# Kernel optimization log

Hardware: AMD Instinct MI355X
Metric: run time of the kernel (lower is better)

## Reference

```python
import jax, jax.numpy as jnp
import numpy as np

B, S, D = 1, 2048, 2048
NH, NKV, HD = 16, 8, 128
FF = 8192
L = 2
V = 32000
THETA = 10000.0
EPS = 1e-5
SCALE = 0.02


def setup_inputs() -> dict:
    key = jax.random.key(0)
    ks = jax.random.split(key, 16)
    return {
        "input_ids": jax.random.randint(ks[0], (B, S), 0, V, dtype=jnp.int32),
        "embed": jax.random.normal(ks[1], (V, D), jnp.float32) * SCALE,
        "Wq": jax.random.normal(ks[2], (L, D, NH * HD), jnp.float32) * SCALE,
        "Wk": jax.random.normal(ks[3], (L, D, NKV * HD), jnp.float32) * SCALE,
        "Wv": jax.random.normal(ks[4], (L, D, NKV * HD), jnp.float32) * SCALE,
        "Wo": jax.random.normal(ks[5], (L, NH * HD, D), jnp.float32) * SCALE,
        "Wgate": jax.random.normal(ks[6], (L, D, FF), jnp.float32) * SCALE,
        "Wup": jax.random.normal(ks[7], (L, D, FF), jnp.float32) * SCALE,
        "Wdown": jax.random.normal(ks[8], (L, FF, D), jnp.float32) * SCALE,
        "norm_attn": jnp.ones((L, D), jnp.float32),
        "norm_mlp": jnp.ones((L, D), jnp.float32),
        "norm_final": jnp.ones((D,), jnp.float32),
        "lm_head": jax.random.normal(ks[9], (D, V), jnp.float32) * SCALE,
        "D1": jax.random.normal(ks[10], (S,), jnp.float32) + 2.0,
        "D2": jax.random.normal(ks[11], (HD,), jnp.float32) + 2.0,
        "D3": jax.random.normal(ks[12], (S,), jnp.float32) + 2.0,
    }


def _rms_norm(x, w):
    return x * jax.lax.rsqrt(jnp.mean(x * x, axis=-1, keepdims=True) + EPS) * w


def _rotate_half(x):
    x1, x2 = jnp.split(x, 2, axis=-1)
    return jnp.concatenate([-x2, x1], axis=-1)


def _forward(input_ids, embed, Wq, Wk, Wv, Wo, Wgate, Wup, Wdown,
             norm_attn, norm_mlp, norm_final, lm_head, D1, D2, D3):
    # RoPE tables: [1,1,S,HD]
    inv_freq = 1.0 / (THETA ** (jnp.arange(0, HD, 2, dtype=jnp.float32) / HD))
    freqs = jnp.arange(S, dtype=jnp.float32)[:, None] * inv_freq[None, :]
    emb = jnp.concatenate([freqs, freqs], axis=-1)
    cos = jnp.cos(emb)[None, None]
    sin = jnp.sin(emb)[None, None]
    causal = jnp.tril(jnp.ones((S, S), dtype=bool))
    neg = jnp.finfo(jnp.float32).min
    D1i, D2i, D3i = 1.0 / D1, 1.0 / D2, 1.0 / D3
    n_rep = NH // NKV

    h = embed[input_ids]  # [B,S,D]
    for l in range(L):
        # --- attention block ---
        x = _rms_norm(h, norm_attn[l])
        q = (x @ Wq[l]).reshape(B, S, NH, HD).transpose(0, 2, 1, 3)   # [B,NH,S,HD]
        k = (x @ Wk[l]).reshape(B, S, NKV, HD).transpose(0, 2, 1, 3)  # [B,NKV,S,HD]
        v = (x @ Wv[l]).reshape(B, S, NKV, HD).transpose(0, 2, 1, 3)
        q = q * cos + _rotate_half(q) * sin
        k = k * cos + _rotate_half(k) * sin
        # repeat_kv (GQA)
        k = jnp.repeat(k, n_rep, axis=1)
        v = jnp.repeat(v, n_rep, axis=1)
        # TEE diagonal encryption: Q' = D1 Q D2, K'^T = D2^-1 K^T D3
        q_enc = q * D1[None, None, :, None] * D2[None, None, None, :]
        k_enc = k * D3[None, None, :, None] * D2i[None, None, None, :]
        scores = jnp.einsum('bhqd,bhkd->bhqk', q_enc, k_enc)
        # decrypt: D1^-1 (Q'K'^T) D3^-1  (mathematically cancels encryption)
        scores = scores * D1i[None, None, :, None] * D3i[None, None, None, :]
        scores = scores / jnp.sqrt(jnp.float32(HD))
        scores = jnp.where(causal[None, None], scores, neg)
        probs = jax.nn.softmax(scores, axis=-1)
        o = jnp.einsum('bhqk,bhkd->bhqd', probs, v)
        o = o.transpose(0, 2, 1, 3).reshape(B, S, NH * HD)
        h = h + o @ Wo[l]
        # --- SwiGLU MLP block ---
        x = _rms_norm(h, norm_mlp[l])
        h = h + (jax.nn.silu(x @ Wgate[l]) * (x @ Wup[l])) @ Wdown[l]

    h = _rms_norm(h, norm_final)
    return h @ lm_head  # logits [B,S,V]


def reference(input_ids, embed, Wq, Wk, Wv, Wo, Wgate, Wup, Wdown,
              norm_attn, norm_mlp, norm_final, lm_head, D1, D2, D3):
    return _forward(input_ids, embed, Wq, Wk, Wv, Wo, Wgate, Wup, Wdown,
                    norm_attn, norm_mlp, norm_final, lm_head, D1, D2, D3)
```

## Files before the change

kernel.cpp:

```cpp
#include <hip/hip_runtime.h>
#include <cstdint>
#include <cstddef>

typedef __attribute__((ext_vector_type(4))) float f32x4;
typedef __attribute__((ext_vector_type(8))) short short8;
typedef __attribute__((ext_vector_type(4))) unsigned int u32x4;

static const int TS = 2048;
static const int DM = 2048;
static const int NHEAD = 16, NKVH = 8, HDIM = 128;
static const int FFD = 8192;
static const int NVOC = 32000;
static const int QKVN = 4096;

__device__ __forceinline__ unsigned short f2bf(float f){
  unsigned int u = __builtin_bit_cast(unsigned int, f);
  u += 0x7FFFu + ((u >> 16) & 1u);
  return (unsigned short)(u >> 16);
}
__device__ __forceinline__ float bf2f(short h){
  unsigned int u = ((unsigned int)(unsigned short)h) << 16;
  return __builtin_bit_cast(float, u);
}
__device__ __forceinline__ f32x4 mfma16(short8 a, short8 b, f32x4 c){
  return __builtin_amdgcn_mfma_f32_16x16x32_bf16(a, b, c, 0, 0, 0);
}
__device__ __forceinline__ void gload16(const void* g, void* l){
  __builtin_amdgcn_global_load_lds(
      (const __attribute__((address_space(1))) unsigned int*)g,
      (__attribute__((address_space(3))) unsigned int*)l, 16, 0, 0);
}

__global__ void rope_tables_k(float* __restrict__ cosT, float* __restrict__ sinT){
  int idx = blockIdx.x * 256 + threadIdx.x;
  int s = idx >> 6, j = idx & 63;
  float inv = exp2f(-(float)j * (13.287712379549449f / 64.0f));
  float ang = (float)s * inv;
  cosT[idx] = cosf(ang);
  sinT[idx] = sinf(ang);
}

__global__ void embed_k(const int* __restrict__ ids, const float* __restrict__ E,
                        float* __restrict__ h){
  int s = blockIdx.x, tid = threadIdx.x;
  long id = ids[s];
  const f32x4* src = (const f32x4*)(E + id * (long)DM);
  f32x4* dst = (f32x4*)(h + (long)s * DM);
  dst[tid] = src[tid];
  dst[tid + 256] = src[tid + 256];
}

__global__ void rmsnorm_k(const float* __restrict__ x, const float* __restrict__ w,
                          short* __restrict__ out){
  int s = blockIdx.x, tid = threadIdx.x;
  const float* row = x + (long)s * DM;
  f32x4 v0 = *(const f32x4*)&row[tid * 8];
  f32x4 v1 = *(const f32x4*)&row[tid * 8 + 4];
  float ss = v0[0]*v0[0] + v0[1]*v0[1] + v0[2]*v0[2] + v0[3]*v0[3]
           + v1[0]*v1[0] + v1[1]*v1[1] + v1[2]*v1[2] + v1[3]*v1[3];
  #pragma unroll
  for (int off = 32; off; off >>= 1) ss += __shfl_xor(ss, off);
  __shared__ float sred[4];
  int wave = tid >> 6, lane = tid & 63;
  if (lane == 0) sred[wave] = ss;
  __syncthreads();
  float tot = sred[0] + sred[1] + sred[2] + sred[3];
  float r = rsqrtf(tot * (1.0f / (float)DM) + 1e-5f);
  f32x4 w0 = *(const f32x4*)&w[tid * 8];
  f32x4 w1 = *(const f32x4*)&w[tid * 8 + 4];
  short8 o;
  #pragma unroll
  for (int j = 0; j < 4; j++) o[j] = (short)f2bf(v0[j] * r * w0[j]);
  #pragma unroll
  for (int j = 0; j < 4; j++) o[4 + j] = (short)f2bf(v1[j] * r * w1[j]);
  *(short8*)&out[(long)s * DM + tid * 8] = o;
}

__global__ void transpose_k(const float* __restrict__ B, short* __restrict__ Bt,
                            int K, int N){
  __shared__ float t[64][65];
  int tid = threadIdx.x;
  int kb = blockIdx.y * 64, nb = blockIdx.x * 64;
  int r0 = tid >> 4, c4 = tid & 15;
  #pragma unroll
  for (int p = 0; p < 4; p++){
    int r = r0 + p * 16;
    f32x4 v = *(const f32x4*)&B[(long)(kb + r) * N + nb + c4 * 4];
    t[r][c4*4+0] = v[0]; t[r][c4*4+1] = v[1]; t[r][c4*4+2] = v[2]; t[r][c4*4+3] = v[3];
  }
  __syncthreads();
  int n0 = tid >> 3, k0 = (tid & 7) * 8;
  #pragma unroll
  for (int p = 0; p < 2; p++){
    int n = n0 + p * 32;
    short8 o;
    #pragma unroll
    for (int j = 0; j < 8; j++) o[j] = (short)f2bf(t[k0 + j][n]);
    *(short8*)&Bt[(long)(nb + n) * K + kb + k0] = o;
  }
}

__global__ void vtrans_k(const short* __restrict__ vb, short* __restrict__ vtb, int stride){
  int s0 = blockIdx.x * 64, kv = blockIdx.y;
  int tid = threadIdx.x;
  int s = s0 + (tid & 63);
  int d0 = (tid >> 6) * 8;
  #pragma unroll
  for (int p = 0; p < 4; p++){
    int d = d0 + p * 32;
    short8 v = *(const short8*)&vb[(long)s * stride + kv * HDIM + d];
    #pragma unroll
    for (int j = 0; j < 8; j++)
      vtb[(long)(kv * HDIM + d + j) * TS + s] = v[j];
  }
}

__global__ void rope_apply_k(short* __restrict__ buf, const float* __restrict__ cosT,
                             const float* __restrict__ sinT, int nh, int stride, int coloff){
  int idx = blockIdx.x * 256 + threadIdx.x;
  int j = idx & 63;
  int t = idx >> 6;
  int hh = t % nh;
  int s = t / nh;
  long base = (long)s * stride + coloff + hh * HDIM + j;
  float c = cosT[s * 64 + j], sn = sinT[s * 64 + j];
  float x1 = bf2f(buf[base]), x2 = bf2f(buf[base + 64]);
  buf[base]      = (short)f2bf(x1 * c - x2 * sn);
  buf[base + 64] = (short)f2bf(x2 * c + x1 * sn);
}

__global__ void reduce4_k(const float* __restrict__ p, float* __restrict__ h){
  const long stride = (long)TS * DM;
  long i = ((long)blockIdx.x * 256 + threadIdx.x) * 4;
  f32x4 a = *(const f32x4*)&h[i];
  f32x4 v0 = *(const f32x4*)&p[i];
  f32x4 v1 = *(const f32x4*)&p[i + stride];
  f32x4 v2 = *(const f32x4*)&p[i + 2 * stride];
  f32x4 v3 = *(const f32x4*)&p[i + 3 * stride];
  a = a + ((v0 + v1) + (v2 + v3));
  *(f32x4*)&h[i] = a;
}

template<int EPI>
__global__ __launch_bounds__(512, 2)
void gemm256(const short* __restrict__ A, int lda,
             const short* __restrict__ Bt, int ldb,
             float* __restrict__ Cf, short* __restrict__ Cb,
             const short* __restrict__ Xtra, int N, int K){
  __shared__ short lds[4][2][8192];
  const int tid = threadIdx.x;
  const int wid = tid >> 6, lane = tid & 63;
  const int wr = wid >> 2, wc = wid & 3;
  const int fr = lane & 15, fch = lane >> 4;
  const int nt = K >> 5;

  const int z = blockIdx.y;
  A  += (long)z * K;
  Bt += (long)z * K;

  const int nbt = N >> 8;
  const int nwg = nbt << 3;
  const int q = nwg >> 3;
  const int swz = (blockIdx.x & 7) * q + (blockIdx.x >> 3);
  const int mb = swz & 7, nb = swz >> 3;

  const short* Abase = A  + (long)(mb * 256 + fr) * lda + fch * 8;
  const short* Bbase = Bt + (long)(nb * 256 + fr) * ldb + fch * 8;
  const int gA0 = wid * 2, gA1 = wid * 2 + 1;

  short8 aE[4], aO[4], bE[2], bO[2];
  f32x4 acc[8][4] = {};

#define STG_A(bufc, g_, tau_) \
  gload16(Abase + (long)((g_) * 16) * lda + (long)(tau_) * 32, &lds[bufc][0][(g_) * 512])
#define STG_B(bufc, g_, tau_) \
  gload16(Bbase + (long)((g_) * 16) * ldb + (long)(tau_) * 32, &lds[bufc][1][(g_) * 512])
#define RDA(dst, bufc, mh) do{ \
    _Pragma("unroll") \
    for (int j_ = 0; j_ < 4; j_++) \
      dst[j_] = *(const short8*)&lds[bufc][0][(wr * 8 + (mh) * 4 + j_) * 512 + fch * 128 + fr * 8]; \
  }while(0)
#define RDB(dst, bufc, nh) do{ \
    _Pragma("unroll") \
    for (int i_ = 0; i_ < 2; i_++) \
      dst[i_] = *(const short8*)&lds[bufc][1][(wc * 4 + (nh) * 2 + i_) * 512 + fch * 128 + fr * 8]; \
  }while(0)
#define MM8(va, vb, mh, nh) do{ \
    __builtin_amdgcn_s_setprio(1); \
    _Pragma("unroll") \
    for (int j_ = 0; j_ < 4; j_++) \
      _Pragma("unroll") \
      for (int i_ = 0; i_ < 2; i_++) \
        acc[(mh)*4+j_][(nh)*2+i_] = mfma16(va[j_], vb[i_], acc[(mh)*4+j_][(nh)*2+i_]); \
    __builtin_amdgcn_s_setprio(0); \
  }while(0)
#define SB __builtin_amdgcn_sched_barrier(0)

#define TILE(t_, bufR, bufN, bufS, bC, bNx) do{ \
    const int tau_ = ((t_) + 2 < nt) ? (t_) + 2 : nt - 1; \
    RDB(bNx, bufR, 1); STG_A(bufS, gA0, tau_); SB; MM8(aE, bC, 0, 0); \
    RDA(aO,  bufR, 1); STG_A(bufS, gA1, tau_); SB; MM8(aE, bNx, 0, 1); \
    asm volatile("s_waitcnt vmcnt(2)" ::: "memory"); \
    __builtin_amdgcn_s_barrier(); \
    RDA(aE,  bufN, 0); STG_B(bufS, gA0, tau_); SB; MM8(aO, bNx, 1, 1); \
    RDB(bNx, bufN, 0); STG_B(bufS, gA1, tau_); SB; MM8(aO, bC, 1, 0); \
    __builtin_amdgcn_s_barrier(); \
  }while(0)

  STG_A(0, gA0, 0); STG_A(0, gA1, 0); STG_B(0, gA0, 0); STG_B(0, gA1, 0);
  STG_A(1, gA0, 1); STG_A(1, gA1, 1); STG_B(1, gA0, 1); STG_B(1, gA1, 1);
  asm volatile("s_waitcnt vmcnt(4)" ::: "memory");
  __builtin_amdgcn_s_barrier();
  RDA(aE, 0, 0); RDB(bE, 0, 0);

  const int nIter = nt >> 2;
  for (int it = 0; it < nIter; ++it){
    const int t0 = it << 2;
    TILE(t0 + 0, 0, 1, 2, bE, bO);
    TILE(t0 + 1, 1, 2, 3, bO, bE);
    TILE(t0 + 2, 2, 3, 0, bE, bO);
    TILE(t0 + 3, 3, 0, 1, bO, bE);
  }

#undef STG_A
#undef STG_B
#undef RDA
#undef RDB
#undef MM8
#undef SB
#undef TILE

  const int rb0 = mb * 256 + wr * 128 + fch * 4;
  const int cb0 = nb * 256 + wc * 64 + fr;
  const long pbase = (EPI == 5) ? (long)z * ((long)TS * N) : 0;
  #pragma unroll
  for (int m = 0; m < 8; m++)
    #pragma unroll
    for (int n = 0; n < 4; n++)
      #pragma unroll
      for (int i = 0; i < 4; i++){
        long idx = (long)(rb0 + m * 16 + i) * N + (cb0 + n * 16);
        float v = acc[m][n][i];
        if constexpr (EPI == 0) Cf[idx] = v;
        else if constexpr (EPI == 1) Cb[idx] = (short)f2bf(v);
        else if constexpr (EPI == 3){
          float sg = 1.0f / (1.0f + __expf(-v));
          Cb[idx] = (short)f2bf(v * sg);
        } else if constexpr (EPI == 4){
          float g = bf2f(Xtra[idx]);
          Cb[idx] = (short)f2bf(g * v);
        } else {
          Cf[pbase + idx] = v;
        }
      }
}

template<int EPI>
__global__ __launch_bounds__(256)
void gemm_bt(const short* __restrict__ A, const short* __restrict__ Bt,
             float* __restrict__ Cf, short* __restrict__ Cb,
             const short* __restrict__ Xtra, int N, int K){
  __shared__ short As[4096];
  __shared__ short Bs[4096];
  const int tid = threadIdx.x;
  const int wave = tid >> 6, lane = tid & 63;
  const int wr = wave >> 1, wc = wave & 1;
  const int mb = blockIdx.y, nb = blockIdx.x;

  const int srow = lane & 15;
  const int scol = (lane >> 4) * 8;
  const short* ApL0 = A + (long)(mb * 128 + wave * 16 + srow) * K + scol;
  const short* ApL1 = ApL0 + (long)64 * K;
  const short* BpL0 = Bt + (long)(nb * 128 + wave * 16 + srow) * K + scol;
  const short* BpL1 = BpL0 + (long)64 * K;

  f32x4 acc[4][4] = {};
  const int fr = lane & 15, fch = lane >> 4;

  for (int kb = 0; kb < K; kb += 32){
    __syncthreads();
    gload16(ApL0 + kb, &As[wave * 512]);
    gload16(ApL1 + kb, &As[(4 + wave) * 512]);
    gload16(BpL0 + kb, &Bs[wave * 512]);
    gload16(BpL1 + kb, &Bs[(4 + wave) * 512]);
    __syncthreads();
    short8 a[4], b[4];
    #pragma unroll
    for (int m = 0; m < 4; m++)
      a[m] = *(const short8*)&As[(wr * 4 + m) * 512 + fch * 128 + fr * 8];
    #pragma unroll
    for (int n = 0; n < 4; n++)
      b[n] = *(const short8*)&Bs[(wc * 4 + n) * 512 + fch * 128 + fr * 8];
    #pragma unroll
    for (int m = 0; m < 4; m++)
      #pragma unroll
      for (int n = 0; n < 4; n++)
        acc[m][n] = mfma16(a[m], b[n], acc[m][n]);
  }

  const int rb = mb * 128 + wr * 64 + (lane >> 4) * 4;
  const int cb = nb * 128 + wc * 64 + (lane & 15);
  #pragma unroll
  for (int m = 0; m < 4; m++)
    #pragma unroll
    for (int n = 0; n < 4; n++)
      #pragma unroll
      for (int i = 0; i < 4; i++){
        long idx = (long)(rb + m * 16 + i) * N + (cb + n * 16);
        float v = acc[m][n][i];
        if constexpr (EPI == 0) Cf[idx] = v;
        else if constexpr (EPI == 1) Cb[idx] = (short)f2bf(v);
        else if constexpr (EPI == 2) Cf[idx] += v;
        else if constexpr (EPI == 3){
          float sg = 1.0f / (1.0f + __expf(-v));
          Cb[idx] = (short)f2bf(v * sg);
        } else {
          float g = bf2f(Xtra[idx]);
          Cb[idx] = (short)f2bf(g * v);
        }
      }
}

__device__ __forceinline__ int qoff(int r, int cB){ return r * 256 + (cB ^ ((r & 7) << 4)); }
__device__ __forceinline__ int voff(int d, int cB){ return d * 128 + (cB ^ ((d & 7) << 4)); }
__device__ __forceinline__ int poff(int r, int cB){ return r * 128 + (cB ^ ((r & 7) << 4)); }

__global__ __launch_bounds__(256)
void attn_k(const short* __restrict__ qb, const short* __restrict__ kb,
            const short* __restrict__ vtb, short* __restrict__ ob){
  __shared__ short Qs[64 * 128];
  __shared__ short Ks[64 * 128];
  __shared__ short Vt[128 * 64];
  __shared__ short Ps[64 * 64];
  const int tid = threadIdx.x, wave = tid >> 6, lane = tid & 63;
  const int qt = blockIdx.x, head = blockIdx.y, kvh = head >> 1;
  const float scale = 0.08838834764831845f;

  {
    int r0 = tid >> 4, c16 = tid & 15;
    #pragma unroll
    for (int p = 0; p < 4; p++){
      int r = r0 + p * 16;
      u32x4 v = *(const u32x4*)&qb[(long)(qt * 64 + r) * QKVN + head * HDIM + c16 * 8];
      *(u32x4*)((char*)Qs + qoff(r, c16 * 16)) = v;
    }
  }

  float mrun[4] = {-1e30f, -1e30f, -1e30f, -1e30f};
  float lrun[4] = {0.f, 0.f, 0.f, 0.f};
  f32x4 accO[8] = {};

  for (int kt = 0; kt <= qt; kt++){
    __syncthreads();
    {
      int r0 = tid >> 4, c16 = tid & 15;
      #pragma unroll
      for (int p = 0; p < 4; p++){
        int r = r0 + p * 16;
        u32x4 v = *(const u32x4*)&kb[(long)(kt * 64 + r) * QKVN + kvh * HDIM + c16 * 8];
        *(u32x4*)((char*)Ks + qoff(r, c16 * 16)) = v;
      }
      int vr0 = tid >> 3, vc = tid & 7;
      #pragma unroll
      for (int p = 0; p < 4; p++){
        int d = vr0 + p * 32;
        u32x4 v = *(const u32x4*)&vtb[(long)(kvh * HDIM + d) * TS + kt * 64 + vc * 8];
        *(u32x4*)((char*)Vt + voff(d, vc * 16)) = v;
      }
    }
    __syncthreads();

    f32x4 sacc[4] = {};
    #pragma unroll
    for (int k4 = 0; k4 < 4; k4++){
      short8 aq = *(const short8*)((const char*)Qs +
                   qoff(wave * 16 + (lane & 15), k4 * 64 + (lane >> 4) * 16));
      #pragma unroll
      for (int n = 0; n < 4; n++){
        short8 bk = *(const short8*)((const char*)Ks +
                     qoff(n * 16 + (lane & 15), k4 * 64 + (lane >> 4) * 16));
        sacc[n] = mfma16(aq, bk, sacc[n]);
      }
    }

    const bool diag = (kt == qt);
    float mt[4] = {-1e30f, -1e30f, -1e30f, -1e30f};
    #pragma unroll
    for (int n = 0; n < 4; n++)
      #pragma unroll
      for (int i = 0; i < 4; i++){
        float v = sacc[n][i] * scale;
        if (diag){
          int rr = (lane >> 4) * 4 + i + wave * 16;
          int cc = n * 16 + (lane & 15);
          if (cc > rr) v = -1e30f;
        }
        sacc[n][i] = v;
        mt[i] = fmaxf(mt[i], v);
      }
    #pragma unroll
    for (int off = 1; off < 16; off <<= 1)
      #pragma unroll
      for (int i = 0; i < 4; i++) mt[i] = fmaxf(mt[i], __shfl_xor(mt[i], off));
    float alpha[4], rsum[4];
    #pragma unroll
    for (int i = 0; i < 4; i++){
      float mn = fmaxf(mrun[i], mt[i]);
      alpha[i] = __expf(mrun[i] - mn);
      mrun[i] = mn;
      rsum[i] = 0.f;
    }
    #pragma unroll
    for (int n = 0; n < 4; n++)
      #pragma unroll
      for (int i = 0; i < 4; i++){
        float p = __expf(sacc[n][i] - mrun[i]);
        sacc[n][i] = p;
        rsum[i] += p;
      }
    #pragma unroll
    for (int off = 1; off < 16; off <<= 1)
      #pragma unroll
      for (int i = 0; i < 4; i++) rsum[i] += __shfl_xor(rsum[i], off);
    #pragma unroll
    for (int i = 0; i < 4; i++) lrun[i] = lrun[i] * alpha[i] + rsum[i];

    #pragma unroll
    for (int n = 0; n < 4; n++)
      #pragma unroll
      for (int i = 0; i < 4; i++){
        int rr = wave * 16 + (lane >> 4) * 4 + i;
        int cc = n * 16 + (lane & 15);
        *(short*)((char*)Ps + poff(rr, cc * 2)) = (short)f2bf(sacc[n][i]);
      }

    #pragma unroll
    for (int n = 0; n < 8; n++)
      #pragma unroll
      for (int i = 0; i < 4; i++) accO[n][i] *= alpha[i];
    #pragma unroll
    for (int ks = 0; ks < 2; ks++){
      short8 ap = *(const short8*)((const char*)Ps +
                   poff(wave * 16 + (lane & 15), ks * 64 + (lane >> 4) * 16));
      #pragma unroll
      for (int n = 0; n < 8; n++){
        short8 bv = *(const short8*)((const char*)Vt +
                     voff(n * 16 + (lane & 15), ks * 64 + (lane >> 4) * 16));
        accO[n] = mfma16(ap, bv, accO[n]);
      }
    }
  }

  #pragma unroll
  for (int i = 0; i < 4; i++){
    float inv = 1.0f / lrun[i];
    int rr = qt * 64 + wave * 16 + (lane >> 4) * 4 + i;
    #pragma unroll
    for (int n = 0; n < 8; n++){
      int cc = head * HDIM + n * 16 + (lane & 15);
      ob[(long)rr * DM + cc] = (short)f2bf(accO[n][i] * inv);
    }
  }
}

extern "C" void kernel_launch(void* const* d_in, const int* in_sizes, int n_in,
                              void* d_out, int out_size, void* d_ws, size_t ws_size,
                              hipStream_t stream){
  (void)in_sizes; (void)n_in; (void)out_size; (void)ws_size;
  const int*   ids = (const int*)d_in[0];
  const float* E   = (const float*)d_in[1];
  const float* Wq  = (const float*)d_in[2];
  const float* Wk  = (const float*)d_in[3];
  const float* Wv  = (const float*)d_in[4];
  const float* Wo  = (const float*)d_in[5];
  const float* Wg  = (const float*)d_in[6];
  const float* Wu  = (const float*)d_in[7];
  const float* Wd  = (const float*)d_in[8];
  const float* nA  = (const float*)d_in[9];
  const float* nM  = (const float*)d_in[10];
  const float* nF  = (const float*)d_in[11];
  const float* LMH = (const float*)d_in[12];
  float* out = (float*)d_out;

  char* ws = (char*)d_ws;
  size_t off = 0;
  auto alloc = [&](size_t bytes){ void* p = ws + off; off += (bytes + 255) & ~(size_t)255; return p; };
  float* h    = (float*)alloc((size_t)TS * DM * 4);
  short* xb   = (short*)alloc((size_t)TS * DM * 2);
  short* qkvb = (short*)alloc((size_t)TS * QKVN * 2);
  short* vtb  = (short*)alloc((size_t)NKVH * HDIM * TS * 2);
  short* obuf = (short*)alloc((size_t)TS * DM * 2);
  short* sg   = (short*)alloc((size_t)TS * FFD * 2);
  short* actb = (short*)alloc((size_t)TS * FFD * 2);
  float* cosT = (float*)alloc((size_t)TS * 64 * 4);
  float* sinT = (float*)alloc((size_t)TS * 64 * 4);
  short* wT   = (short*)alloc((size_t)NVOC * DM * 2);
  float* pPart = (float*)((char*)wT + (size_t)36 * 1024 * 1024);

  rope_tables_k<<<512, 256, 0, stream>>>(cosT, sinT);
  embed_k<<<TS, 256, 0, stream>>>(ids, E, h);

  for (int l = 0; l < 2; l++){
    rmsnorm_k<<<TS, 256, 0, stream>>>(h, nA + (size_t)l * DM, xb);
    transpose_k<<<dim3(32, 32), 256, 0, stream>>>(Wq + (size_t)l * DM * DM, wT, DM, DM);
    transpose_k<<<dim3(16, 32), 256, 0, stream>>>(Wk + (size_t)l * DM * 1024, wT + (size_t)2048 * DM, DM, 1024);
    transpose_k<<<dim3(16, 32), 256, 0, stream>>>(Wv + (size_t)l * DM * 1024, wT + (size_t)3072 * DM, DM, 1024);
    gemm256<1><<<dim3(128), 512, 0, stream>>>(xb, DM, wT, DM, nullptr, qkvb, nullptr, QKVN, DM);
    rope_apply_k<<<8192, 256, 0, stream>>>(qkvb, cosT, sinT, NHEAD, QKVN, 0);
    rope_apply_k<<<4096, 256, 0, stream>>>(qkvb, cosT, sinT, NKVH, QKVN, 2048);
    vtrans_k<<<dim3(32, 8), 256, 0, stream>>>(qkvb + 3072, vtb, QKVN);
    attn_k<<<dim3(32, 16), 256, 0, stream>>>(qkvb, qkvb + 2048, vtb, obuf);
    transpose_k<<<dim3(32, 32), 256, 0, stream>>>(Wo + (size_t)l * DM * DM, wT, DM, DM);
    gemm_bt<2><<<dim3(16, 16), 256, 0, stream>>>(obuf, wT, h, nullptr, nullptr, DM, DM);
    rmsnorm_k<<<TS, 256, 0, stream>>>(h, nM + (size_t)l * DM, xb);
    transpose_k<<<dim3(128, 32), 256, 0, stream>>>(Wg + (size_t)l * DM * FFD, wT, DM, FFD);
    gemm256<3><<<dim3(256), 512, 0, stream>>>(xb, DM, wT, DM, nullptr, sg, nullptr, FFD, DM);
    transpose_k<<<dim3(128, 32), 256, 0, stream>>>(Wu + (size_t)l * DM * FFD, wT, DM, FFD);
    gemm256<4><<<dim3(256), 512, 0, stream>>>(xb, DM, wT, DM, nullptr, actb, sg, FFD, DM);
    transpose_k<<<dim3(32, 128), 256, 0, stream>>>(Wd + (size_t)l * FFD * DM, wT, FFD, DM);
    gemm256<5><<<dim3(64, 4), 512, 0, stream>>>(actb, FFD, wT, FFD, pPart, nullptr, nullptr, DM, FFD / 4);
    reduce4_k<<<4096, 256, 0, stream>>>(pPart, h);
  }

  rmsnorm_k<<<TS, 256, 0, stream>>>(h, nF, xb);
  transpose_k<<<dim3(500, 32), 256, 0, stream>>>(LMH, wT, DM, NVOC);
  gemm256<0><<<dim3(1000), 512, 0, stream>>>(xb, DM, wT, DM, out, nullptr, nullptr, NVOC, DM);
}
```

Before: 1.546 ms.

## Store GEMM operands in pre-tiled 16x32 bf16 blocks for contiguous loads

Adds a tiled offset function so activations (rmsnorm output, attention output, SwiGLU product) and transposed weights are written as contiguous 16x32 bf16 tiles. The GEMM kernels then load each tile with one fully contiguous 1KB wave-wide global_load_lds instead of 16 strided row segments. This aims to improve global memory coalescing and cut TLB and address-computation cost in the main GEMMs. In exchange, producer stores become scattered in the tiled layout, and every consumer must agree on the layout.

```diff
diff --git a/kernel.cpp b/kernel.cpp
--- a/kernel.cpp
+++ b/kernel.cpp
@@ -29,6 +29,10 @@
   __builtin_amdgcn_global_load_lds(
       (const __attribute__((address_space(1))) unsigned int*)g,
       (__attribute__((address_space(3))) unsigned int*)l, 16, 0, 0);
+}
+__device__ __forceinline__ long toff(int r, int k, int ldk){
+  return ((long)((r >> 4) * ldk + (k >> 5)) << 9)
+       + (((k & 31) >> 3) << 7) + ((r & 15) << 3) + (k & 7);
 }
 
 __global__ void rope_tables_k(float* __restrict__ cosT, float* __restrict__ sinT){
@@ -73,7 +77,7 @@
   for (int j = 0; j < 4; j++) o[j] = (short)f2bf(v0[j] * r * w0[j]);
   #pragma unroll
   for (int j = 0; j < 4; j++) o[4 + j] = (short)f2bf(v1[j] * r * w1[j]);
-  *(short8*)&out[(long)s * DM + tid * 8] = o;
+  *(short8*)&out[toff(s, tid * 8, DM >> 5)] = o;
 }
 
 __global__ void transpose_k(const float* __restrict__ B, short* __restrict__ Bt,
@@ -82,6 +86,7 @@
   int tid = threadIdx.x;
   int kb = blockIdx.y * 64, nb = blockIdx.x * 64;
   int r0 = tid >> 4, c4 = tid & 15;
+  const int ldk = K >> 5;
   #pragma unroll
   for (int p = 0; p < 4; p++){
     int r = r0 + p * 16;
@@ -96,7 +101,7 @@
     short8 o;
     #pragma unroll
     for (int j = 0; j < 8; j++) o[j] = (short)f2bf(t[k0 + j][n]);
-    *(short8*)&Bt[(long)(nb + n) * K + kb + k0] = o;
+    *(short8*)&Bt[toff(nb + n, kb + k0, ldk)] = o;
   }
 }
 
@@ -143,10 +148,10 @@
 
 template<int EPI>
 __global__ __launch_bounds__(512, 2)
-void gemm256(const short* __restrict__ A, int lda,
-             const short* __restrict__ Bt, int ldb,
+void gemm256(const short* __restrict__ A, int ldkA,
+             const short* __restrict__ Bt, int ldkB,
              float* __restrict__ Cf, short* __restrict__ Cb,
-             const short* __restrict__ Xtra, int N, int K){
+             const short* __restrict__ Xtra, int N, int K, int ldkC){
   __shared__ short lds[4][2][8192];
   const int tid = threadIdx.x;
   const int wid = tid >> 6, lane = tid & 63;
@@ -155,8 +160,7 @@
   const int nt = K >> 5;
 
   const int z = blockIdx.y;
-  A  += (long)z * K;
-  Bt += (long)z * K;
+  const int k0 = z * nt;
 
   const int nbt = N >> 8;
   const int nwg = nbt << 3;
@@ -164,17 +168,17 @@
   const int swz = (blockIdx.x & 7) * q + (blockIdx.x >> 3);
   const int mb = swz & 7, nb = swz >> 3;
 
-  const short* Abase = A  + (long)(mb * 256 + fr) * lda + fch * 8;
-  const short* Bbase = Bt + (long)(nb * 256 + fr) * ldb + fch * 8;
+  const short* Abase = A  + ((long)(mb * 16) * ldkA + k0) * 512 + lane * 8;
+  const short* Bbase = Bt + ((long)(nb * 16) * ldkB + k0) * 512 + lane * 8;
   const int gA0 = wid * 2, gA1 = wid * 2 + 1;
 
   short8 aE[4], aO[4], bE[2], bO[2];
   f32x4 acc[8][4] = {};
 
 #define STG_A(bufc, g_, tau_) \
-  gload16(Abase + (long)((g_) * 16) * lda + (long)(tau_) * 32, &lds[bufc][0][(g_) * 512])
+  gload16(Abase + ((long)(g_) * ldkA + (tau_)) * 512, &lds[bufc][0][(g_) * 512])
 #define STG_B(bufc, g_, tau_) \
-  gload16(Bbase + (long)((g_) * 16) * ldb + (long)(tau_) * 32, &lds[bufc][1][(g_) * 512])
+  gload16(Bbase + ((long)(g_) * ldkB + (tau_)) * 512, &lds[bufc][1][(g_) * 512])
 #define RDA(dst, bufc, mh) do{ \
     _Pragma("unroll") \
     for (int j_ = 0; j_ < 4; j_++) \
@@ -239,7 +243,8 @@
     for (int n = 0; n < 4; n++)
       #pragma unroll
       for (int i = 0; i < 4; i++){
-        long idx = (long)(rb0 + m * 16 + i) * N + (cb0 + n * 16);
+        const int rr = rb0 + m * 16 + i, cc = cb0 + n * 16;
+        long idx = (long)rr * N + cc;
         float v = acc[m][n][i];
         if constexpr (EPI == 0) Cf[idx] = v;
         else if constexpr (EPI == 1) Cb[idx] = (short)f2bf(v);
@@ -248,7 +253,7 @@
           Cb[idx] = (short)f2bf(v * sg);
         } else if constexpr (EPI == 4){
           float g = bf2f(Xtra[idx]);
-          Cb[idx] = (short)f2bf(g * v);
+          Cb[toff(rr, cc, ldkC)] = (short)f2bf(g * v);
         } else {
           Cf[pbase + idx] = v;
         }
@@ -257,7 +262,8 @@
 
 template<int EPI>
 __global__ __launch_bounds__(256)
-void gemm_bt(const short* __restrict__ A, const short* __restrict__ Bt,
+void gemm_bt(const short* __restrict__ A, int ldkA,
+             const short* __restrict__ Bt, int ldkB,
              float* __restrict__ Cf, short* __restrict__ Cb,
              const short* __restrict__ Xtra, int N, int K){
   __shared__ short As[4096];
@@ -267,22 +273,19 @@
   const int wr = wave >> 1, wc = wave & 1;
   const int mb = blockIdx.y, nb = blockIdx.x;
 
-  const int srow = lane & 15;
-  const int scol = (lane >> 4) * 8;
-  const short* ApL0 = A + (long)(mb * 128 + wave * 16 + srow) * K + scol;
-  const short* ApL1 = ApL0 + (long)64 * K;
-  const short* BpL0 = Bt + (long)(nb * 128 + wave * 16 + srow) * K + scol;
-  const short* BpL1 = BpL0 + (long)64 * K;
+  const short* Abase = A  + (long)(mb * 8) * ldkA * 512 + lane * 8;
+  const short* Bbase = Bt + (long)(nb * 8) * ldkB * 512 + lane * 8;
 
   f32x4 acc[4][4] = {};
   const int fr = lane & 15, fch = lane >> 4;
-
-  for (int kb = 0; kb < K; kb += 32){
+  const int nt = K >> 5;
+
+  for (int tau = 0; tau < nt; tau++){
     __syncthreads();
-    gload16(ApL0 + kb, &As[wave * 512]);
-    gload16(ApL1 + kb, &As[(4 + wave) * 512]);
-    gload16(BpL0 + kb, &Bs[wave * 512]);
-    gload16(BpL1 + kb, &Bs[(4 + wave) * 512]);
+    gload16(Abase + ((long)wave * ldkA + tau) * 512,       &As[wave * 512]);
+    gload16(Abase + ((long)(wave + 4) * ldkA + tau) * 512, &As[(4 + wave) * 512]);
+    gload16(Bbase + ((long)wave * ldkB + tau) * 512,       &Bs[wave * 512]);
+    gload16(Bbase + ((long)(wave + 4) * ldkB + tau) * 512, &Bs[(4 + wave) * 512]);
     __syncthreads();
     short8 a[4], b[4];
     #pragma unroll
@@ -458,7 +461,7 @@
     #pragma unroll
     for (int n = 0; n < 8; n++){
       int cc = head * HDIM + n * 16 + (lane & 15);
-      ob[(long)rr * DM + cc] = (short)f2bf(accO[n][i] * inv);
+      ob[toff(rr, cc, DM >> 5)] = (short)f2bf(accO[n][i] * inv);
     }
   }
 }
@@ -505,24 +508,24 @@
     transpose_k<<<dim3(32, 32), 256, 0, stream>>>(Wq + (size_t)l * DM * DM, wT, DM, DM);
     transpose_k<<<dim3(16, 32), 256, 0, stream>>>(Wk + (size_t)l * DM * 1024, wT + (size_t)2048 * DM, DM, 1024);
     transpose_k<<<dim3(16, 32), 256, 0, stream>>>(Wv + (size_t)l * DM * 1024, wT + (size_t)3072 * DM, DM, 1024);
-    gemm256<1><<<dim3(128), 512, 0, stream>>>(xb, DM, wT, DM, nullptr, qkvb, nullptr, QKVN, DM);
+    gemm256<1><<<dim3(128), 512, 0, stream>>>(xb, 64, wT, 64, nullptr, qkvb, nullptr, QKVN, DM, 0);
     rope_apply_k<<<8192, 256, 0, stream>>>(qkvb, cosT, sinT, NHEAD, QKVN, 0);
     rope_apply_k<<<4096, 256, 0, stream>>>(qkvb, cosT, sinT, NKVH, QKVN, 2048);
     vtrans_k<<<dim3(32, 8), 256, 0, stream>>>(qkvb + 3072, vtb, QKVN);
     attn_k<<<dim3(32, 16), 256, 0, stream>>>(qkvb, qkvb + 2048, vtb, obuf);
     transpose_k<<<dim3(32, 32), 256, 0, stream>>>(Wo + (size_t)l * DM * DM, wT, DM, DM);
-    gemm_bt<2><<<dim3(16, 16), 256, 0, stream>>>(obuf, wT, h, nullptr, nullptr, DM, DM);
+    gemm_bt<2><<<dim3(16, 16), 256, 0, stream>>>(obuf, 64, wT, 64, h, nullptr, nullptr, DM, DM);
     rmsnorm_k<<<TS, 256, 0, stream>>>(h, nM + (size_t)l * DM, xb);
     transpose_k<<<dim3(128, 32), 256, 0, stream>>>(Wg + (size_t)l * DM * FFD, wT, DM, FFD);
-    gemm256<3><<<dim3(256), 512, 0, stream>>>(xb, DM, wT, DM, nullptr, sg, nullptr, FFD, DM);
+    gemm256<3><<<dim3(256), 512, 0, stream>>>(xb, 64, wT, 64, nullptr, sg, nullptr, FFD, DM, 0);
     transpose_k<<<dim3(128, 32), 256, 0, stream>>>(Wu + (size_t)l * DM * FFD, wT, DM, FFD);
-    gemm256<4><<<dim3(256), 512, 0, stream>>>(xb, DM, wT, DM, nullptr, actb, sg, FFD, DM);
+    gemm256<4><<<dim3(256), 512, 0, stream>>>(xb, 64, wT, 64, nullptr, actb, sg, FFD, DM, FFD >> 5);
     transpose_k<<<dim3(32, 128), 256, 0, stream>>>(Wd + (size_t)l * FFD * DM, wT, FFD, DM);
-    gemm256<5><<<dim3(64, 4), 512, 0, stream>>>(actb, FFD, wT, FFD, pPart, nullptr, nullptr, DM, FFD / 4);
+    gemm256<5><<<dim3(64, 4), 512, 0, stream>>>(actb, 256, wT, 256, pPart, nullptr, nullptr, DM, FFD / 4, 0);
     reduce4_k<<<4096, 256, 0, stream>>>(pPart, h);
   }
 
   rmsnorm_k<<<TS, 256, 0, stream>>>(h, nF, xb);
   transpose_k<<<dim3(500, 32), 256, 0, stream>>>(LMH, wT, DM, NVOC);
-  gemm256<0><<<dim3(1000), 512, 0, stream>>>(xb, DM, wT, DM, out, nullptr, nullptr, NVOC, DM);
-}
+  gemm256<0><<<dim3(1000), 512, 0, stream>>>(xb, 64, wT, 64, out, nullptr, nullptr, NVOC, DM, 0);
+}
```

New measurement: 1.403 ms. 1.1x faster.
